# Kernel tuning notes

Measured on AMD Instinct MI355X. Metric: run time of the kernel, lower is better.

The kernel has to match this reference:

```python
import jax, jax.numpy as jnp
import numpy as np

C1, C2, BIG_K, STRIDE = 256, 256, 13, 1
EPS = 1e-5  # BatchNorm2d default


def setup_inputs() -> dict:
    key = jax.random.key(0)
    k1, k2, k3, k4, k5 = jax.random.split(key, 5)
    x = jax.random.normal(k1, (16, C1, 56, 56), dtype=jnp.float32)
    # Conv2d weight: (out_ch, in_ch, kH, kW), kaiming-ish scale
    w = jax.random.normal(k2, (C2, C1, BIG_K, BIG_K), dtype=jnp.float32) * (1.0 / np.sqrt(C1 * BIG_K * BIG_K))
    gamma = jax.random.uniform(k3, (C2,), dtype=jnp.float32, minval=0.5, maxval=1.5)
    beta = jax.random.normal(k4, (C2,), dtype=jnp.float32) * 0.1
    running_mean = jnp.zeros((C2,), dtype=jnp.float32)
    running_var = jax.random.uniform(k5, (C2,), dtype=jnp.float32, minval=0.5, maxval=1.5)
    return {"x": x, "w": w, "gamma": gamma, "beta": beta,
            "running_mean": running_mean, "running_var": running_var}


def reference(x, w, gamma, beta, running_mean, running_var):
    # Dense big_k x big_k conv fallback: Conv2d(c1, c2, 13, stride=1, pad=6, bias=False)
    pad = BIG_K // 2
    y = jax.lax.conv_general_dilated(
        x, w,
        window_strides=(STRIDE, STRIDE),
        padding=[(pad, pad), (pad, pad)],
        dimension_numbers=("NCHW", "OIHW", "NCHW"),
    )
    # BatchNorm2d (inference mode: running stats)
    inv = jax.lax.rsqrt(running_var + EPS)
    y = (y - running_mean[None, :, None, None]) * (gamma * inv)[None, :, None, None] + beta[None, :, None, None]
    # SiLU activation
    return y * jax.nn.sigmoid(y)
```

## Files before the change

### kernel.cpp

```cpp
#include <hip/hip_runtime.h>
#include <hip/hip_bf16.h>

#define C1c 256
#define C2c 256
#define NBAT 16
#define HH 56
#define WW 56
#define KS 13
#define PADc 6
#define HP 68
#define NPIX (NBAT*HH*WW)
#define PIXTILES 224
#define PTILE 224
#define KSTEPS2 1352

typedef __bf16 bf16;
typedef bf16 bf16x8 __attribute__((ext_vector_type(8)));
typedef float floatx4 __attribute__((ext_vector_type(4)));

#define XT_ELEMS ((size_t)NBAT*HP*HP*C1c)
#define WT_ELEMS ((size_t)KSTEPS2*256*32)

__global__ __launch_bounds__(256) void xform_x(const float* __restrict__ x,
                                               bf16* __restrict__ xT) {
  __shared__ bf16 tile[56][258];
  const int tid = threadIdx.x;
  const int n = blockIdx.x / HP;
  const int hp = blockIdx.x - n * HP;
  const int ih = hp - PADc;
  const size_t pos_base = (size_t)(n * HP + hp) * HP * C1c;

  if (ih < 0 || ih >= HH) {
#pragma unroll 1
    for (int i = tid; i < HP * 32; i += 256) {
      int wp = i >> 5, g = i & 31;
      *(uint4*)(xT + pos_base + wp * C1c + g * 8) = (uint4){0u, 0u, 0u, 0u};
    }
    return;
  }

  const int wave = tid >> 6, lane = tid & 63;
#pragma unroll 4
  for (int i = 0; i < 64; ++i) {
    int c = i * 4 + wave;
    if (lane < WW) {
      float v = x[(((size_t)n * C1c + c) * HH + ih) * WW + lane];
      tile[lane][c] = (bf16)v;
    }
  }
  __syncthreads();

#pragma unroll 1
  for (int i = tid; i < HP * 32; i += 256) {
    int wp = i >> 5, g = i & 31;
    int iw = wp - PADc;
    uint4 o;
    if (iw >= 0 && iw < WW) {
      const uint* lp = (const uint*)&tile[iw][g * 8];
      o.x = lp[0]; o.y = lp[1]; o.z = lp[2]; o.w = lp[3];
    } else {
      o = (uint4){0u, 0u, 0u, 0u};
    }
    *(uint4*)(xT + pos_base + wp * C1c + g * 8) = o;
  }
}

__global__ __launch_bounds__(256) void xform_w(const float* __restrict__ w,
                                               bf16* __restrict__ wT) {
  int j = blockIdx.x * 256 + threadIdx.x;
  int part = j & 3;
  int c2 = (j >> 2) & 255;
  int kk = j >> 10;
  int kw = kk % 13;
  int t = kk / 13;
  int q = t & 7;
  int kh = t >> 3;
  int c1 = q * 32 + part * 8;
  const float* wp = w + ((size_t)c2 * C1c + c1) * (KS * KS) + kh * KS + kw;
  bf16x8 v;
#pragma unroll
  for (int i = 0; i < 8; i++) v[i] = (bf16)wp[(size_t)i * KS * KS];
  *(bf16x8*)(wT + (size_t)j * 8) = v;
}

__device__ __forceinline__ void gload_lds16(const bf16* g, bf16* l) {
  __builtin_amdgcn_global_load_lds(
      (const __attribute__((address_space(1))) void*)(g),
      (__attribute__((address_space(3))) void*)(l),
      16, 0, 0);
}

__global__ __launch_bounds__(512, 2) void conv_mfma(
    const bf16* __restrict__ xT, const bf16* __restrict__ wT,
    const float* __restrict__ gamma, const float* __restrict__ beta,
    const float* __restrict__ rmean, const float* __restrict__ rvar,
    float* __restrict__ out) {
  __shared__ __attribute__((aligned(16))) bf16 As[3][256 * 32];
  __shared__ __attribute__((aligned(16))) bf16 Bs[3][PTILE * 32];
  __shared__ float sS[256];
  __shared__ float sB[256];

  const int tid = threadIdx.x;
  const int lane = tid & 63;
  const int wave = tid >> 6;
  const int wm = wave >> 1, wn = wave & 1;

  const int orig = blockIdx.x;
  const int pixt = (orig & 7) * 28 + (orig >> 3);
  const int pixbase = pixt * PTILE;

  if (tid < 256) {
    float s = gamma[tid] * rsqrtf(rvar[tid] + 1e-5f);
    sS[tid] = s;
    sB[tid] = beta[tid] - rmean[tid] * s;
  }
  __syncthreads();

  const int part = tid & 3;
  const int row0 = tid >> 2;
  const int srcg = (part ^ ((row0 >> 1) & 3)) * 8;

  const int aOff0 = row0 * 32 + srcg;
  const int aOff1 = aOff0 + 128 * 32;

  const bool bstage = (wave < 7);
  int pOff0 = 0, pOff1 = 0;
  if (bstage) {
    int pix = pixbase + row0;
    int n = pix / (HH * WW);
    int rr = pix - n * (HH * WW);
    int oh = rr / WW;
    int ow = rr - oh * WW;
    pOff0 = ((n * HP + oh) * HP + ow) * C1c + srcg;
    pix += 112;
    n = pix / (HH * WW);
    rr = pix - n * (HH * WW);
    oh = rr / WW;
    ow = rr - oh * WW;
    pOff1 = ((n * HP + oh) * HP + ow) * C1c + srcg;
  }

  const int ldsA0 = wave * 512;
  const int ldsB1 = 112 * 32 + wave * 512;

  const int mrow = lane & 15;
  const int kq = lane >> 4;
  const int g0 = (kq ^ ((mrow >> 1) & 3)) * 8;
  const int aRB = (wm * 64 + mrow) * 32 + g0;
  const int bRB = (wn * 112 + mrow) * 32 + g0;

  floatx4 acc[4][7];
#pragma unroll
  for (int mi = 0; mi < 4; mi++)
#pragma unroll
    for (int ni = 0; ni < 7; ni++) acc[mi][ni] = (floatx4){0.f, 0.f, 0.f, 0.f};

  gload_lds16(wT + aOff0, &As[0][ldsA0]);
  gload_lds16(wT + aOff1, &As[0][4096 + ldsA0]);
  if (bstage) {
    gload_lds16(xT + pOff0, &Bs[0][ldsA0]);
    gload_lds16(xT + pOff1, &Bs[0][ldsB1]);
  }
  gload_lds16(wT + 8192 + aOff0, &As[1][ldsA0]);
  gload_lds16(wT + 8192 + aOff1, &As[1][4096 + ldsA0]);
  if (bstage) {
    gload_lds16(xT + pOff0 + C1c, &Bs[1][ldsA0]);
    gload_lds16(xT + pOff1 + C1c, &Bs[1][ldsB1]);
  }
  if (bstage) { asm volatile("s_waitcnt vmcnt(4)" ::: "memory"); }
  else        { asm volatile("s_waitcnt vmcnt(2)" ::: "memory"); }
  __builtin_amdgcn_s_barrier();

  int kwn = 2, qn = 0, khn = 0;
  const bf16* aPre = wT + 2 * 8192;

  auto do_step = [&](const bf16* Ac, const bf16* Bc, bf16* An, bf16* Bn) {
    bf16x8 af[4], bfr[7];
#pragma unroll
    for (int mi = 0; mi < 2; mi++)
      af[mi] = *(const bf16x8*)(Ac + aRB + mi * 512);
#pragma unroll
    for (int ni = 0; ni < 7; ni++)
      bfr[ni] = *(const bf16x8*)(Bc + bRB + ni * 512);
    gload_lds16(aPre + aOff0, An + ldsA0);
    gload_lds16(aPre + aOff1, An + 4096 + ldsA0);
    __builtin_amdgcn_sched_barrier(0);
    __builtin_amdgcn_s_barrier();
    __builtin_amdgcn_sched_barrier(0);
    __builtin_amdgcn_s_setprio(1);
#pragma unroll
    for (int mi = 0; mi < 2; mi++)
#pragma unroll
      for (int ni = 0; ni < 7; ni++)
        acc[mi][ni] = __builtin_amdgcn_mfma_f32_16x16x32_bf16(
            af[mi], bfr[ni], acc[mi][ni], 0, 0, 0);
    __builtin_amdgcn_s_setprio(0);

#pragma unroll
    for (int mi = 2; mi < 4; mi++)
      af[mi] = *(const bf16x8*)(Ac + aRB + mi * 512);
    int bOn = (khn * HP + kwn) * C1c + qn * 32;
    if (bstage) {
      gload_lds16(xT + pOff0 + bOn, Bn + ldsA0);
      gload_lds16(xT + pOff1 + bOn, Bn + ldsB1);
    }
    kwn++; aPre += 8192;
    if (kwn == 13) {
      kwn = 0; qn++;
      if (qn == 8) {
        qn = 0; khn++;
        if (khn == 13) { khn = 0; aPre = wT; }
      }
    }
    __builtin_amdgcn_sched_barrier(0);
    __builtin_amdgcn_s_barrier();
    __builtin_amdgcn_sched_barrier(0);
    __builtin_amdgcn_s_setprio(1);
#pragma unroll
    for (int mi = 2; mi < 4; mi++)
#pragma unroll
      for (int ni = 0; ni < 7; ni++)
        acc[mi][ni] = __builtin_amdgcn_mfma_f32_16x16x32_bf16(
            af[mi], bfr[ni], acc[mi][ni], 0, 0, 0);
    __builtin_amdgcn_s_setprio(0);

    if (bstage) { asm volatile("s_waitcnt vmcnt(4)" ::: "memory"); }
    else        { asm volatile("s_waitcnt vmcnt(2)" ::: "memory"); }
    __builtin_amdgcn_s_barrier();
  };

#pragma unroll 1
  for (int kk = 0; kk < KSTEPS2 - 2; kk += 3) {
    do_step(As[0], Bs[0], As[2], Bs[2]);
    do_step(As[1], Bs[1], As[0], Bs[0]);
    do_step(As[2], Bs[2], As[1], Bs[1]);
  }
  do_step(As[0], Bs[0], As[2], Bs[2]);
  do_step(As[1], Bs[1], As[0], Bs[0]);

  const int colL = lane & 15;
  const int quad = lane >> 4;
#pragma unroll
  for (int ni = 0; ni < 7; ni++) {
    int pix = pixbase + wn * 112 + ni * 16 + colL;
    int n = pix / (HH * WW);
    int rr = pix - n * (HH * WW);
    int oh = rr / WW;
    int ow = rr - oh * WW;
    size_t obase = (size_t)n * C2c * (HH * WW) + (size_t)oh * WW + ow;
#pragma unroll
    for (int mi = 0; mi < 4; mi++) {
      int rowb = wm * 64 + mi * 16 + quad * 4;
#pragma unroll
      for (int r = 0; r < 4; r++) {
        int rowl = rowb + r;
        float v = acc[mi][ni][r];
        v = v * sS[rowl] + sB[rowl];
        float o = v / (1.f + __expf(-v));
        out[obase + (size_t)rowl * (HH * WW)] = o;
      }
    }
  }
}

extern "C" void kernel_launch(void* const* d_in, const int* in_sizes, int n_in,
                              void* d_out, int out_size, void* d_ws, size_t ws_size,
                              hipStream_t stream) {
  const float* x     = (const float*)d_in[0];
  const float* w     = (const float*)d_in[1];
  const float* gamma = (const float*)d_in[2];
  const float* beta  = (const float*)d_in[3];
  const float* rmean = (const float*)d_in[4];
  const float* rvar  = (const float*)d_in[5];
  float* out = (float*)d_out;

  bf16* xT = (bf16*)d_ws;
  bf16* wT = xT + XT_ELEMS;

  if (ws_size < (XT_ELEMS + WT_ELEMS) * sizeof(bf16)) return;

  xform_x<<<NBAT * HP, 256, 0, stream>>>(x, xT);
  xform_w<<<(KSTEPS2 * 256 * 4) / 256, 256, 0, stream>>>(w, wT);
  conv_mfma<<<PIXTILES, 512, 0, stream>>>(xT, wT, gamma, beta, rmean, rvar, out);
}
```

Before: 1.217 ms.

## Drop LDS staging and load MFMA operands directly from global memory

Removes the triple-buffered LDS pipeline (global_load_lds, barriers, swizzled LDS reads) and has each wave load its A and B fragments straight from global memory (L2/L1) on every K step. This gets rid of barrier synchronisation and LDS traffic. In exchange there is no cross-wave data reuse through LDS and no software prefetch, so every step waits on global load latency and global/L2 traffic goes up a lot.

Result: slower. 2.843 ms (+133.7%).

```diff
diff --git a/kernel.cpp b/kernel.cpp
--- a/kernel.cpp
+++ b/kernel.cpp
@@ -83,20 +83,11 @@
   *(bf16x8*)(wT + (size_t)j * 8) = v;
 }
 
-__device__ __forceinline__ void gload_lds16(const bf16* g, bf16* l) {
-  __builtin_amdgcn_global_load_lds(
-      (const __attribute__((address_space(1))) void*)(g),
-      (__attribute__((address_space(3))) void*)(l),
-      16, 0, 0);
-}
-
 __global__ __launch_bounds__(512, 2) void conv_mfma(
     const bf16* __restrict__ xT, const bf16* __restrict__ wT,
     const float* __restrict__ gamma, const float* __restrict__ beta,
     const float* __restrict__ rmean, const float* __restrict__ rvar,
     float* __restrict__ out) {
-  __shared__ __attribute__((aligned(16))) bf16 As[3][256 * 32];
-  __shared__ __attribute__((aligned(16))) bf16 Bs[3][PTILE * 32];
   __shared__ float sS[256];
   __shared__ float sB[256];
 
@@ -116,38 +107,20 @@
   }
   __syncthreads();
 
-  const int part = tid & 3;
-  const int row0 = tid >> 2;
-  const int srcg = (part ^ ((row0 >> 1) & 3)) * 8;
-
-  const int aOff0 = row0 * 32 + srcg;
-  const int aOff1 = aOff0 + 128 * 32;
-
-  const bool bstage = (wave < 7);
-  int pOff0 = 0, pOff1 = 0;
-  if (bstage) {
-    int pix = pixbase + row0;
+  const int mrow = lane & 15;
+  const int kq = lane >> 4;
+  const int aLane = (wm * 64 + mrow) * 32 + kq * 8;
+
+  int pBe[7];
+#pragma unroll
+  for (int ni = 0; ni < 7; ni++) {
+    int pix = pixbase + wn * 112 + ni * 16 + mrow;
     int n = pix / (HH * WW);
     int rr = pix - n * (HH * WW);
     int oh = rr / WW;
     int ow = rr - oh * WW;
-    pOff0 = ((n * HP + oh) * HP + ow) * C1c + srcg;
-    pix += 112;
-    n = pix / (HH * WW);
-    rr = pix - n * (HH * WW);
-    oh = rr / WW;
-    ow = rr - oh * WW;
-    pOff1 = ((n * HP + oh) * HP + ow) * C1c + srcg;
-  }
-
-  const int ldsA0 = wave * 512;
-  const int ldsB1 = 112 * 32 + wave * 512;
-
-  const int mrow = lane & 15;
-  const int kq = lane >> 4;
-  const int g0 = (kq ^ ((mrow >> 1) & 3)) * 8;
-  const int aRB = (wm * 64 + mrow) * 32 + g0;
-  const int bRB = (wn * 112 + mrow) * 32 + g0;
+    pBe[ni] = ((n * HP + oh) * HP + ow) * C1c + kq * 8;
+  }
 
   floatx4 acc[4][7];
 #pragma unroll
@@ -155,88 +128,39 @@
 #pragma unroll
     for (int ni = 0; ni < 7; ni++) acc[mi][ni] = (floatx4){0.f, 0.f, 0.f, 0.f};
 
-  gload_lds16(wT + aOff0, &As[0][ldsA0]);
-  gload_lds16(wT + aOff1, &As[0][4096 + ldsA0]);
-  if (bstage) {
-    gload_lds16(xT + pOff0, &Bs[0][ldsA0]);
-    gload_lds16(xT + pOff1, &Bs[0][ldsB1]);
-  }
-  gload_lds16(wT + 8192 + aOff0, &As[1][ldsA0]);
-  gload_lds16(wT + 8192 + aOff1, &As[1][4096 + ldsA0]);
-  if (bstage) {
-    gload_lds16(xT + pOff0 + C1c, &Bs[1][ldsA0]);
-    gload_lds16(xT + pOff1 + C1c, &Bs[1][ldsB1]);
-  }
-  if (bstage) { asm volatile("s_waitcnt vmcnt(4)" ::: "memory"); }
-  else        { asm volatile("s_waitcnt vmcnt(2)" ::: "memory"); }
-  __builtin_amdgcn_s_barrier();
-
-  int kwn = 2, qn = 0, khn = 0;
-  const bf16* aPre = wT + 2 * 8192;
-
-  auto do_step = [&](const bf16* Ac, const bf16* Bc, bf16* An, bf16* Bn) {
+  const bf16* aCur = wT;
+  int kwc = 0, qc = 0;
+  int bOn = 0;
+
+#pragma unroll 1
+  for (int t = 0; t < KSTEPS2; ++t) {
     bf16x8 af[4], bfr[7];
 #pragma unroll
-    for (int mi = 0; mi < 2; mi++)
-      af[mi] = *(const bf16x8*)(Ac + aRB + mi * 512);
+    for (int mi = 0; mi < 4; mi++)
+      af[mi] = *(const bf16x8*)(aCur + aLane + mi * 512);
+    const bf16* xb = xT + bOn;
 #pragma unroll
     for (int ni = 0; ni < 7; ni++)
-      bfr[ni] = *(const bf16x8*)(Bc + bRB + ni * 512);
-    gload_lds16(aPre + aOff0, An + ldsA0);
-    gload_lds16(aPre + aOff1, An + 4096 + ldsA0);
-    __builtin_amdgcn_sched_barrier(0);
-    __builtin_amdgcn_s_barrier();
-    __builtin_amdgcn_sched_barrier(0);
+      bfr[ni] = *(const bf16x8*)(xb + pBe[ni]);
+
     __builtin_amdgcn_s_setprio(1);
 #pragma unroll
-    for (int mi = 0; mi < 2; mi++)
-#pragma unroll
-      for (int ni = 0; ni < 7; ni++)
+    for (int ni = 0; ni < 7; ni++)
+#pragma unroll
+      for (int mi = 0; mi < 4; mi++)
         acc[mi][ni] = __builtin_amdgcn_mfma_f32_16x16x32_bf16(
             af[mi], bfr[ni], acc[mi][ni], 0, 0, 0);
     __builtin_amdgcn_s_setprio(0);
 
-#pragma unroll
-    for (int mi = 2; mi < 4; mi++)
-      af[mi] = *(const bf16x8*)(Ac + aRB + mi * 512);
-    int bOn = (khn * HP + kwn) * C1c + qn * 32;
-    if (bstage) {
-      gload_lds16(xT + pOff0 + bOn, Bn + ldsA0);
-      gload_lds16(xT + pOff1 + bOn, Bn + ldsB1);
-    }
-    kwn++; aPre += 8192;
-    if (kwn == 13) {
-      kwn = 0; qn++;
-      if (qn == 8) {
-        qn = 0; khn++;
-        if (khn == 13) { khn = 0; aPre = wT; }
+    aCur += 8192;
+    kwc++; bOn += C1c;
+    if (kwc == KS) {
+      kwc = 0; qc++; bOn += 32 - KS * C1c;
+      if (qc == 8) {
+        qc = 0; bOn += HP * C1c - 8 * 32;
       }
     }
-    __builtin_amdgcn_sched_barrier(0);
-    __builtin_amdgcn_s_barrier();
-    __builtin_amdgcn_sched_barrier(0);
-    __builtin_amdgcn_s_setprio(1);
-#pragma unroll
-    for (int mi = 2; mi < 4; mi++)
-#pragma unroll
-      for (int ni = 0; ni < 7; ni++)
-        acc[mi][ni] = __builtin_amdgcn_mfma_f32_16x16x32_bf16(
-            af[mi], bfr[ni], acc[mi][ni], 0, 0, 0);
-    __builtin_amdgcn_s_setprio(0);
-
-    if (bstage) { asm volatile("s_waitcnt vmcnt(4)" ::: "memory"); }
-    else        { asm volatile("s_waitcnt vmcnt(2)" ::: "memory"); }
-    __builtin_amdgcn_s_barrier();
-  };
-
-#pragma unroll 1
-  for (int kk = 0; kk < KSTEPS2 - 2; kk += 3) {
-    do_step(As[0], Bs[0], As[2], Bs[2]);
-    do_step(As[1], Bs[1], As[0], Bs[0]);
-    do_step(As[2], Bs[2], As[1], Bs[1]);
-  }
-  do_step(As[0], Bs[0], As[2], Bs[2]);
-  do_step(As[1], Bs[1], As[0], Bs[0]);
+  }
 
   const int colL = lane & 15;
   const int quad = lane >> 4;
```
